# Kernel tuning notes

Hardware: AMD Instinct MI355X
Metric: run time of the kernel (lower is better)

## Reference

```python
import jax, jax.numpy as jnp
import numpy as np


def _linear_interp(t, S):
    """1D linear interpolation along last axis, matching F.interpolate(mode='linear', align_corners=False).
    t: [B, C, L] -> [B, C, S]"""
    L = t.shape[-1]
    src = jnp.clip((jnp.arange(S, dtype=jnp.float32) + 0.5) * (L / S) - 0.5, 0.0, L - 1)
    i0 = jnp.floor(src).astype(jnp.int32)
    i1 = jnp.minimum(i0 + 1, L - 1)
    w = (src - i0.astype(jnp.float32)).astype(t.dtype)
    return t[..., i0] * (1.0 - w) + t[..., i1] * w


def setup_inputs() -> dict:
    key = jax.random.key(0)
    k1, k2, k3, k4 = jax.random.split(key, 4)
    B, C, H, W, L, D = 32, 768, 32, 32, 77, 512
    return {
        "img_feat": jax.random.normal(k1, (B, C, H, W), dtype=jnp.float32),
        "text_feat": jax.random.normal(k2, (B, L, D), dtype=jnp.float32),
        "W_txt": jax.random.normal(k3, (D, C), dtype=jnp.float32) / np.float32(np.sqrt(D)),
        "gamma": jax.random.normal(k4, (1,), dtype=jnp.float32) * 0.1,
    }


def reference(img_feat, text_feat, W_txt, gamma):
    B, C, H, W = img_feat.shape
    S = H * W
    q = img_feat.reshape(B, C, S)                          # [B,C,S]
    # Linear(D->C, bias=False) then transpose(1,2): [B,L,D] -> [B,C,L]
    t = jnp.einsum('bld,dc->bcl', text_feat, W_txt)
    t = _linear_interp(t, S)                               # [B,C,S]
    scale = S ** (-0.5)
    # attn = bmm(q [B,C,S], t^T [B,S,C]) * scale -> [B,C,C] channel attention
    attn = jax.nn.softmax(jnp.einsum('bis,bjs->bij', q, t) * scale, axis=-1)
    out = q + gamma * jnp.einsum('bij,bjs->bis', attn, t)  # gamma-gated residual
    return out.reshape(B, C, H, W)
```

## Files before the change

kernel.cpp:

```cpp
#include <hip/hip_runtime.h>

#define BB 32
#define CC 768
#define SS 1024
#define LLn 77
#define DD 512
#define LP 80
#define LP2 96

#define RATIO 0.0751953125f
#define IRATIO 13.298701f

#define CVT_TXT_BLOCKS (BB * LP * DD / 4 / 256)
#define CVT_W_BLOCKS ((CC / 32) * (DD / 32))
#define WT_BLOCKS 14
#define TG_BLOCKS (BB * 5 * 4)
#define QH_BLOCKS (256 * BB)
#define ATTN_BLOCKS (48 * BB)

typedef short bf16x8 __attribute__((ext_vector_type(8)));
typedef float f32x4 __attribute__((ext_vector_type(4)));
typedef unsigned short u16;
typedef unsigned int u32;

#define MFMA __builtin_amdgcn_mfma_f32_16x16x32_bf16

__device__ __forceinline__ u16 f2bf(float f) {
    u32 u; __builtin_memcpy(&u, &f, 4);
    u += 0x7fffu + ((u >> 16) & 1u);
    return (u16)(u >> 16);
}

__device__ __forceinline__ int win_base(int l) {
    int s_lo = max(0, (int)floorf(((float)l - 0.5f) * IRATIO - 0.5f) - 1);
    int base = s_lo & ~3;
    return min(base, SS - 36);
}

__global__ __launch_bounds__(256) void k_cvt(const float* __restrict__ text,
                                             const float* __restrict__ Wt,
                                             u16* __restrict__ At,
                                             u16* __restrict__ Wb,
                                             float* __restrict__ wtab_g) {
    __shared__ float tile[32 * 33];
    const int bx = blockIdx.x;
    const int tid = threadIdx.x;
    if (bx < CVT_TXT_BLOCKS) {
        int j = bx * 256 + tid;
        int row80 = j >> 7, col4 = (j & 127) << 2;
        int b = row80 / LP, l = row80 - b * LP;
        u16 o[4] = {0, 0, 0, 0};
        if (l < LLn) {
            float4 v = *reinterpret_cast<const float4*>(&text[((size_t)b * LLn + l) * DD + col4]);
            o[0] = f2bf(v.x); o[1] = f2bf(v.y); o[2] = f2bf(v.z); o[3] = f2bf(v.w);
        }
        *reinterpret_cast<uint2*>(&At[(size_t)row80 * DD + col4]) = *reinterpret_cast<uint2*>(o);
    } else if (bx < CVT_TXT_BLOCKS + CVT_W_BLOCKS) {
        const int bw = bx - CVT_TXT_BLOCKS;
        const int c0 = (bw % (CC / 32)) * 32, d0 = (bw / (CC / 32)) * 32;
        const int tx = tid & 31, ty = tid >> 5;
#pragma unroll
        for (int k = 0; k < 4; ++k) {
            int d = ty + k * 8;
            tile[d * 33 + tx] = Wt[(size_t)(d0 + d) * CC + c0 + tx];
        }
        __syncthreads();
#pragma unroll
        for (int k = 0; k < 4; ++k) {
            int c = ty + k * 8;
            Wb[(size_t)(c0 + c) * DD + d0 + tx] = f2bf(tile[tx * 33 + c]);
        }
    } else {
        int idx = (bx - CVT_TXT_BLOCKS - CVT_W_BLOCKS) * 256 + tid;
        if (idx < 96 * 36) {
            int l = idx / 36, j = idx - l * 36;
            float wgt = 0.f;
            if (l < LLn) {
                int s = win_base(l) + j;
                float src = fmaf((float)s + 0.5f, RATIO, -0.5f);
                src = fminf(fmaxf(src, 0.f), 76.f);
                wgt = fmaxf(0.f, 1.f - fabsf(src - (float)l));
            }
            wtab_g[l * 36 + j] = wgt;
        }
    }
}

__global__ __launch_bounds__(256) void k_mid(const float* __restrict__ q,
                                             const u16* __restrict__ At,
                                             const u16* __restrict__ Wb,
                                             const float* __restrict__ wtab_g,
                                             u16* __restrict__ qh,
                                             u16* __restrict__ tc,
                                             u16* __restrict__ tlc) {
    const int bx = blockIdx.x;
    const int tid = threadIdx.x;

    if (bx < TG_BLOCKS) {
        const int cg = bx / 160, mt = bx % 160;
        const int b = mt / 5, tile = mt % 5;
        const int l0 = tile * 16;
        const int w = tid >> 6, lane = tid & 63;
        const int lm = lane & 15, lg = lane >> 4;
        const int c0 = cg * 192 + w * 48;

        f32x4 acc[3];
#pragma unroll
        for (int nt = 0; nt < 3; ++nt) acc[nt] = (f32x4){0.f, 0.f, 0.f, 0.f};

        const u16* ap = At + ((size_t)b * LP + l0 + lm) * DD + lg * 8;
        const u16* bp = Wb + (size_t)(c0 + lm) * DD + lg * 8;
#pragma unroll 4
        for (int ks = 0; ks < 16; ++ks) {
            bf16x8 aq = *reinterpret_cast<const bf16x8*>(ap + ks * 32);
#pragma unroll
            for (int nt = 0; nt < 3; ++nt) {
                bf16x8 bv = *reinterpret_cast<const bf16x8*>(bp + (size_t)nt * 16 * DD + ks * 32);
                acc[nt] = MFMA(aq, bv, acc[nt], 0, 0, 0);
            }
        }

        const int lq = l0 + lg * 4;
#pragma unroll
        for (int nt = 0; nt < 3; ++nt) {
            int c = c0 + nt * 16 + lm;
            u16 pk[4];
#pragma unroll
            for (int r = 0; r < 4; ++r) pk[r] = f2bf(acc[nt][r]);
            uint2 pv; __builtin_memcpy(&pv, pk, 8);
            *reinterpret_cast<uint2*>(&tc[((size_t)b * CC + c) * LP2 + lq]) = pv;
#pragma unroll
            for (int r = 0; r < 4; ++r)
                tlc[((size_t)b * LP + lq + r) * CC + c] = pk[r];
        }
        if (tile == 4 && lg == 0) {
            uint4 z = {0u, 0u, 0u, 0u};
#pragma unroll
            for (int nt = 0; nt < 3; ++nt) {
                int c = c0 + nt * 16 + lm;
                *reinterpret_cast<uint4*>(&tc[((size_t)b * CC + c) * LP2 + 80]) = z;
                *reinterpret_cast<uint4*>(&tc[((size_t)b * CC + c) * LP2 + 88]) = z;
            }
        }
    } else {
        const int bxq = bx - TG_BLOCKS;
        const int b = bxq >> 8;
        const int c0 = (bxq & 255) * 3;
#pragma unroll
        for (int k = 0; k < 2; ++k) {
            int idx = tid + (k << 8);
            if (idx >= 3 * LP2) break;
            int r = idx / LP2, l = idx - r * LP2;
            u16 o = 0;
            if (l < LLn) {
                const int base = win_base(l);
                const f32x4* qp = reinterpret_cast<const f32x4*>(
                    &q[((size_t)b * CC + c0 + r) * SS + base]);
                const f32x4* wp = reinterpret_cast<const f32x4*>(&wtab_g[l * 36]);
                f32x4 qv[9], wv[9];
#pragma unroll
                for (int j = 0; j < 9; ++j) { qv[j] = qp[j]; wv[j] = wp[j]; }
                float a = 0.f;
#pragma unroll
                for (int j = 0; j < 9; ++j) {
#pragma unroll
                    for (int e = 0; e < 4; ++e)
                        a = fmaf(qv[j][e], wv[j][e], a);
                }
                o = f2bf(a * 0.03125f);
            }
            qh[((size_t)b * CC + c0 + r) * LP2 + l] = o;
        }
    }
}

__global__ __launch_bounds__(256, 2) void k_attn_out(const u16* __restrict__ qh,
                                                     const u16* __restrict__ tc,
                                                     const u16* __restrict__ tlc,
                                                     const float* __restrict__ q,
                                                     const float* __restrict__ gamma,
                                                     float* __restrict__ out) {
    __shared__ float pmax[4][16];
    __shared__ float psum[4][16];
    __shared__ float us[16 * 80];
    __shared__ __align__(16) char pbuf[4][6400];

    const int id = blockIdx.x;
    const int o = id >> 3;
    const int b = (id & 7) * 4 + o / 48;
    const int iBase = (o % 48) * 16;
    const int tid = threadIdx.x;
    const int w = tid >> 6, lane = tid & 63;
    const int lm = lane & 15, lg = lane >> 4;
    const float g = gamma[0];

    const u16* qbase = qh + ((size_t)b * CC + iBase + lm) * LP2 + lg * 8;
    bf16x8 aq0 = *reinterpret_cast<const bf16x8*>(qbase);
    bf16x8 aq1 = *reinterpret_cast<const bf16x8*>(qbase + 32);
    bf16x8 aq2 = *reinterpret_cast<const bf16x8*>(qbase + 64);

    f32x4 acc[12];
#pragma unroll
    for (int t = 0; t < 12; ++t) acc[t] = (f32x4){0.f, 0.f, 0.f, 0.f};

    const u16* tcb = tc + ((size_t)b * CC + w * 192 + lm) * LP2 + lg * 8;
#pragma unroll
    for (int t = 0; t < 12; ++t) {
        const u16* p = tcb + (size_t)t * 16 * LP2;
        bf16x8 b0 = *reinterpret_cast<const bf16x8*>(p);
        bf16x8 b1 = *reinterpret_cast<const bf16x8*>(p + 32);
        bf16x8 b2 = *reinterpret_cast<const bf16x8*>(p + 64);
        acc[t] = MFMA(aq0, b0, acc[t], 0, 0, 0);
        acc[t] = MFMA(aq1, b1, acc[t], 0, 0, 0);
        acc[t] = MFMA(aq2, b2, acc[t], 0, 0, 0);
    }

    const size_t qBase = ((size_t)b * CC + iBase) * SS + (size_t)(tid << 2);
    f32x4 qreg[16];
#pragma unroll
    for (int r = 0; r < 16; ++r)
        qreg[r] = *reinterpret_cast<const f32x4*>(&q[qBase + (size_t)r * SS]);

    float m[4];
#pragma unroll
    for (int r = 0; r < 4; ++r) {
        float mm = acc[0][r];
#pragma unroll
        for (int t = 1; t < 12; ++t) mm = fmaxf(mm, acc[t][r]);
#pragma unroll
        for (int off = 8; off >= 1; off >>= 1) mm = fmaxf(mm, __shfl_xor(mm, off));
        m[r] = mm;
    }
    if (lm == 0) {
#pragma unroll
        for (int r = 0; r < 4; ++r) pmax[w][lg * 4 + r] = m[r];
    }
    __syncthreads();
    float gm[4];
#pragma unroll
    for (int r = 0; r < 4; ++r) {
        int row = lg * 4 + r;
        gm[r] = fmaxf(fmaxf(pmax[0][row], pmax[1][row]), fmaxf(pmax[2][row], pmax[3][row]));
    }
    float s[4] = {0.f, 0.f, 0.f, 0.f};
#pragma unroll
    for (int t = 0; t < 12; ++t) {
#pragma unroll
        for (int r = 0; r < 4; ++r) {
            float e = __expf(acc[t][r] - gm[r]);
            acc[t][r] = e;
            s[r] += e;
        }
    }
#pragma unroll
    for (int r = 0; r < 4; ++r) {
#pragma unroll
        for (int off = 8; off >= 1; off >>= 1) s[r] += __shfl_xor(s[r], off);
    }
    if (lm == 0) {
#pragma unroll
        for (int r = 0; r < 4; ++r) psum[w][lg * 4 + r] = s[r];
    }

    u16* P = (u16*)pbuf[w];
#pragma unroll
    for (int t = 0; t < 12; ++t) {
#pragma unroll
        for (int r = 0; r < 4; ++r)
            P[(lg * 4 + r) * 200 + t * 16 + lm] = f2bf(acc[t][r]);
    }

    f32x4 u[5];
#pragma unroll
    for (int nt = 0; nt < 5; ++nt) u[nt] = (f32x4){0.f, 0.f, 0.f, 0.f};
    const u16* tb = tlc + ((size_t)b * LP + lm) * CC + w * 192 + lg * 8;
#pragma unroll
    for (int ks = 0; ks < 6; ++ks) {
        bf16x8 pa = *reinterpret_cast<const bf16x8*>(&P[lm * 200 + ks * 32 + lg * 8]);
#pragma unroll
        for (int nt = 0; nt < 5; ++nt) {
            bf16x8 bv = *reinterpret_cast<const bf16x8*>(tb + (size_t)nt * 16 * CC + ks * 32);
            u[nt] = MFMA(pa, bv, u[nt], 0, 0, 0);
        }
    }

    float* up = (float*)pbuf[w];
#pragma unroll
    for (int nt = 0; nt < 5; ++nt) {
#pragma unroll
        for (int r = 0; r < 4; ++r)
            up[(lg * 4 + r) * 81 + nt * 16 + lm] = u[nt][r];
    }
    __syncthreads();
#pragma unroll
    for (int k = 0; k < 5; ++k) {
        int idx = tid + (k << 8);
        int row = idx / LP, l = idx - row * LP;
        float v = ((float*)pbuf[0])[row * 81 + l] + ((float*)pbuf[1])[row * 81 + l]
                + ((float*)pbuf[2])[row * 81 + l] + ((float*)pbuf[3])[row * 81 + l];
        float denom = psum[0][row] + psum[1][row] + psum[2][row] + psum[3][row];
        us[row * LP + l] = v / denom;
    }
    __syncthreads();

    const int s0 = tid << 2;
    float wgt[4]; int i0k[4], i1x[4];
#pragma unroll
    for (int k = 0; k < 4; ++k) {
        float src = fmaf((float)(s0 + k) + 0.5f, RATIO, -0.5f);
        src = fminf(fmaxf(src, 0.f), 76.f);
        i0k[k] = (int)src;
        wgt[k] = src - (float)i0k[k];
        i1x[k] = (i0k[k] < 76) ? i0k[k] + 1 : 76;
    }
#pragma unroll
    for (int r = 0; r < 16; ++r) {
        const float* ur = &us[r * LP];
        f32x4 ov;
#pragma unroll
        for (int k = 0; k < 4; ++k) {
            float uv = fmaf(1.f - wgt[k], ur[i0k[k]], wgt[k] * ur[i1x[k]]);
            ov[k] = qreg[r][k] + g * uv;
        }
        __builtin_nontemporal_store(ov, reinterpret_cast<f32x4*>(&out[qBase + (size_t)r * SS]));
    }
}

extern "C" void kernel_launch(void* const* d_in, const int* in_sizes, int n_in,
                              void* d_out, int out_size, void* d_ws, size_t ws_size,
                              hipStream_t stream) {
    const float* img   = (const float*)d_in[0];
    const float* text  = (const float*)d_in[1];
    const float* Wt    = (const float*)d_in[2];
    const float* gamma = (const float*)d_in[3];
    float* out = (float*)d_out;
    char* ws = (char*)d_ws;
    u16*   tc_bf  = (u16*)(ws);
    u16*   tlc_bf = (u16*)(ws + 4718592);
    u16*   qh_bf  = (u16*)(ws + 8650752);
    u16*   At_bf  = (u16*)(ws + 13369344);
    u16*   Wb_bf  = (u16*)(ws + 15990784);
    float* wtab_g = (float*)(ws + 16777216);

    k_cvt<<<dim3(CVT_TXT_BLOCKS + CVT_W_BLOCKS + WT_BLOCKS), 256, 0, stream>>>(
        text, Wt, At_bf, Wb_bf, wtab_g);
    k_mid<<<dim3(TG_BLOCKS + QH_BLOCKS), 256, 0, stream>>>(
        img, At_bf, Wb_bf, wtab_g, qh_bf, tc_bf, tlc_bf);
    k_attn_out<<<dim3(ATTN_BLOCKS), 256, 0, stream>>>(qh_bf, tc_bf, tlc_bf, img, gamma, out);
}
```

Measured before the change: 108.2 us.

## Stage q tile in LDS as bf16 for qh window reductions

The qh part of k_mid now has each block load a 16-channel by 1024-position q tile with coalesced float4 reads, convert it to bf16 and store it in shared memory. The windowed interpolation dot products then read from LDS instead of issuing scattered global loads per output, and the block count drops from 256 to 48 per batch to match the larger tile. This cuts redundant global traffic on q but adds about 33KB of LDS per block, which shares a kernel with the text-GEMM blocks and may lower their occupancy. It also rounds q to bf16 before the reduction, a small precision change.

```diff
diff --git a/kernel.cpp b/kernel.cpp
--- a/kernel.cpp
+++ b/kernel.cpp
@@ -7,6 +7,7 @@
 #define DD 512
 #define LP 80
 #define LP2 96
+#define QROW 1040
 
 #define RATIO 0.0751953125f
 #define IRATIO 13.298701f
@@ -15,7 +16,7 @@
 #define CVT_W_BLOCKS ((CC / 32) * (DD / 32))
 #define WT_BLOCKS 14
 #define TG_BLOCKS (BB * 5 * 4)
-#define QH_BLOCKS (256 * BB)
+#define QH_BLOCKS (48 * BB)
 #define ATTN_BLOCKS (48 * BB)
 
 typedef short bf16x8 __attribute__((ext_vector_type(8)));
@@ -25,6 +26,10 @@
 
 #define MFMA __builtin_amdgcn_mfma_f32_16x16x32_bf16
 
+__device__ __forceinline__ float bf2f(u32 h16) {
+    u32 u = h16 << 16;
+    float f; __builtin_memcpy(&f, &u, 4); return f;
+}
 __device__ __forceinline__ u16 f2bf(float f) {
     u32 u; __builtin_memcpy(&u, &f, 4);
     u += 0x7fffu + ((u >> 16) & 1u);
@@ -93,6 +98,7 @@
                                              u16* __restrict__ qh,
                                              u16* __restrict__ tc,
                                              u16* __restrict__ tlc) {
+    __shared__ __align__(16) u16 qlds[16 * QROW];
     const int bx = blockIdx.x;
     const int tid = threadIdx.x;
 
@@ -143,33 +149,47 @@
             }
         }
     } else {
-        const int bxq = bx - TG_BLOCKS;
-        const int b = bxq >> 8;
-        const int c0 = (bxq & 255) * 3;
-#pragma unroll
-        for (int k = 0; k < 2; ++k) {
+        const int id = bx - TG_BLOCKS;
+        const int o = id >> 3;
+        const int b = (id & 7) * 4 + o / 48;
+        const int iBase = (o % 48) * 16;
+
+        const size_t qBase = ((size_t)b * CC + iBase) * SS + (size_t)(tid << 2);
+        f32x4 qv[16];
+#pragma unroll
+        for (int r = 0; r < 16; ++r)
+            qv[r] = *reinterpret_cast<const f32x4*>(&q[qBase + (size_t)r * SS]);
+
+#pragma unroll
+        for (int r = 0; r < 16; ++r) {
+            u16 pk[4] = {f2bf(qv[r][0]), f2bf(qv[r][1]), f2bf(qv[r][2]), f2bf(qv[r][3])};
+            uint2 pv; __builtin_memcpy(&pv, pk, 8);
+            *reinterpret_cast<uint2*>(&qlds[r * QROW + (tid << 2)]) = pv;
+        }
+        __syncthreads();
+
+#pragma unroll
+        for (int k = 0; k < 6; ++k) {
             int idx = tid + (k << 8);
-            if (idx >= 3 * LP2) break;
             int r = idx / LP2, l = idx - r * LP2;
-            u16 o = 0;
+            u16 o2 = 0;
             if (l < LLn) {
                 const int base = win_base(l);
-                const f32x4* qp = reinterpret_cast<const f32x4*>(
-                    &q[((size_t)b * CC + c0 + r) * SS + base]);
+                const u16* qrow = &qlds[r * QROW + base];
                 const f32x4* wp = reinterpret_cast<const f32x4*>(&wtab_g[l * 36]);
-                f32x4 qv[9], wv[9];
-#pragma unroll
-                for (int j = 0; j < 9; ++j) { qv[j] = qp[j]; wv[j] = wp[j]; }
                 float a = 0.f;
 #pragma unroll
-                for (int j = 0; j < 9; ++j) {
-#pragma unroll
-                    for (int e = 0; e < 4; ++e)
-                        a = fmaf(qv[j][e], wv[j][e], a);
+                for (int m = 0; m < 9; ++m) {
+                    uint2 hv = *reinterpret_cast<const uint2*>(&qrow[m * 4]);
+                    f32x4 wv = wp[m];
+                    a = fmaf(bf2f(hv.x & 0xffffu), wv[0], a);
+                    a = fmaf(bf2f(hv.x >> 16),     wv[1], a);
+                    a = fmaf(bf2f(hv.y & 0xffffu), wv[2], a);
+                    a = fmaf(bf2f(hv.y >> 16),     wv[3], a);
                 }
-                o = f2bf(a * 0.03125f);
+                o2 = f2bf(a * 0.03125f);
             }
-            qh[((size_t)b * CC + c0 + r) * LP2 + l] = o;
+            qh[((size_t)b * CC + iBase + r) * LP2 + l] = o2;
         }
     }
 }
```

New measurement: 99.25 us. -8.3%, faster.
